# Performance work log

Measured on AMD Instinct MI355X. Metric: run time of the kernel, lower is better.

Reference implementation:

```python
import jax, jax.numpy as jnp
import numpy as np

S = 8192  # query length
T = 8192  # key/value length
D = 256   # head dim


def setup_inputs() -> dict:
    key = jax.random.key(0)
    kq, kk, kv = jax.random.split(key, 3)
    return {
        "query": jax.random.normal(kq, (S, D), dtype=jnp.float32),
        "key": jax.random.normal(kk, (T, D), dtype=jnp.float32),
        "value": jax.random.normal(kv, (T, D), dtype=jnp.float32),
    }


def reference(query, key, value):
    # attn_weights = Q @ K^T  (contract last dims, no batch dims)  -> [S, T]
    attn_weights = jnp.einsum("sd,td->st", query, key)
    # SoftmaxAttn: softmax over axes [ndim//2, ndim) == last axis for 2D
    attn_weights = jax.nn.softmax(attn_weights, axis=-1).astype(jnp.float32)
    # y = A @ V  -> [S, D]
    y = jnp.einsum("st,td->sd", attn_weights, value)
    return y
```

## Files before the change

kernel.cpp:

```cpp
#include <hip/hip_runtime.h>
#include <hip/hip_fp16.h>

#define S_LEN 8192
#define T_LEN 8192
#define D_DIM 256
#define QBLK 128
#define KVBLK 32
#define TSPLIT 8
#define NKV ((T_LEN / TSPLIT) / KVBLK)
#define NQT (S_LEN / QBLK)
#define KTILE_BYTES 16384
#define VTILE_BYTES 16384
#define RESCALE_THR 6.0f
#define LOG2E 1.44269504f
#define SMEM_BYTES 65536

typedef _Float16 f16x8 __attribute__((ext_vector_type(8)));
typedef float f32x4 __attribute__((ext_vector_type(4)));

struct h4 { _Float16 h[4]; };

#define GLOAD_LDS16(g, l)                                              \
    __builtin_amdgcn_global_load_lds(                                  \
        (const __attribute__((address_space(1))) void*)(g),            \
        (__attribute__((address_space(3))) void*)(l), 16, 0, 0)

#define MFMA16(a, b, c) __builtin_amdgcn_mfma_f32_16x16x32_f16(a, b, c, 0, 0, 0)

#if __has_builtin(__builtin_amdgcn_exp2f)
#define EXP2(x) __builtin_amdgcn_exp2f(x)
#else
static __device__ __forceinline__ float EXP2(float x) {
    float y;
    asm("v_exp_f32 %0, %1" : "=v"(y) : "v"(x));
    return y;
}
#endif

__global__ __launch_bounds__(256) void cvt_kernel(const float* __restrict__ in,
                                                  _Float16* __restrict__ out, int n4) {
    int i = blockIdx.x * 256 + threadIdx.x;
    if (i < n4) {
        float4 v = ((const float4*)in)[i];
        h4 o;
        o.h[0] = (_Float16)(v.x * LOG2E); o.h[1] = (_Float16)(v.y * LOG2E);
        o.h[2] = (_Float16)(v.z * LOG2E); o.h[3] = (_Float16)(v.w * LOG2E);
        ((h4*)out)[i] = o;
    }
}

__global__ __launch_bounds__(256) void cvt_swz_kernel(const float* __restrict__ in,
                                                      _Float16* __restrict__ img,
                                                      int nchunks) {
    int id = blockIdx.x * 256 + threadIdx.x;
    if (id >= nchunks) return;
    int row = id >> 5, gr = id & 31;
    int t = row >> 5, r = row & 31;
    float4 a = *(const float4*)(in + (size_t)row * D_DIM + gr * 8);
    float4 b = *(const float4*)(in + (size_t)row * D_DIM + gr * 8 + 4);
    f16x8 o;
    o[0] = (_Float16)a.x; o[1] = (_Float16)a.y; o[2] = (_Float16)a.z; o[3] = (_Float16)a.w;
    o[4] = (_Float16)b.x; o[5] = (_Float16)b.y; o[6] = (_Float16)b.z; o[7] = (_Float16)b.w;
    *(f16x8*)((char*)img + (size_t)t * KTILE_BYTES + (gr >> 2) * 2048 +
              ((r >> 4) << 10) + ((r & 15) << 6) + ((gr & 3) << 4)) = o;
}

__global__ __launch_bounds__(256) void vt_swz_kernel(const float* __restrict__ V,
                                                     _Float16* __restrict__ Vimg) {
    __shared__ float tile[32][260];
    const int t = blockIdx.x;
#pragma unroll
    for (int i = 0; i < 8; ++i) {
        int idx = i * 256 + threadIdx.x;
        int kr = idx >> 6, c4 = idx & 63;
        float4 v = *(const float4*)(V + ((size_t)t * 32 + kr) * D_DIM + c4 * 4);
        tile[kr][c4 * 4 + 0] = v.x;
        tile[kr][c4 * 4 + 1] = v.y;
        tile[kr][c4 * 4 + 2] = v.z;
        tile[kr][c4 * 4 + 3] = v.w;
    }
    __syncthreads();
#pragma unroll
    for (int i = 0; i < 4; ++i) {
        int gid = i * 256 + threadIdx.x;
        int d = gid >> 2, gk = gid & 3;
        f16x8 o;
#pragma unroll
        for (int j = 0; j < 8; ++j)
            o[j] = (_Float16)tile[(j >> 2) * 16 + gk * 4 + (j & 3)][d];
        *(f16x8*)((char*)Vimg + (size_t)t * VTILE_BYTES + ((d >> 4) << 10) +
                  (gk << 8) + ((d & 15) << 4)) = o;
    }
}

__global__ __launch_bounds__(256, 2) void attn_kernel(
    const _Float16* __restrict__ Qh, const _Float16* __restrict__ Kimg,
    const _Float16* __restrict__ Vimg, _Float16* __restrict__ Opart,
    float* __restrict__ ml) {
    extern __shared__ __align__(16) char smem[];
    char* sK = smem;
    char* sV = smem + 32768;
    const int tid = threadIdx.x;
    const int wave = tid >> 6, lane = tid & 63;
    const int g = lane >> 4, c = lane & 15;
    const int bid = blockIdx.x;
    const int qtile = bid >> 3, split = bid & 7;
    const int tile0 = split * NKV;
    const int rot = ((qtile >> 5) << 4) | ((qtile & 3) << 2);
    const int othr = tid * 16;
    const int kbase = ((lane & 15) << 6) | ((lane >> 4) << 4);
    const int vbase = lane << 4;

#define TILE_AT(k) (tile0 + (((k) + rot) & (NKV - 1)))
#define STAGE_KV(k, slot)                                                          \
    {                                                                              \
        const char* Kt = (const char*)Kimg + (size_t)TILE_AT(k) * KTILE_BYTES;     \
        const char* Vt = (const char*)Vimg + (size_t)TILE_AT(k) * VTILE_BYTES;     \
        _Pragma("unroll") for (int i = 0; i < 4; ++i) {                            \
            GLOAD_LDS16(Kt + i * 4096 + othr, sK + (slot)*16384 + i * 4096 + othr); \
            GLOAD_LDS16(Vt + i * 4096 + othr, sV + (slot)*16384 + i * 4096 + othr); \
        }                                                                          \
    }

    f16x8 qf[2][8];
    {
        const size_t qrow0 = (size_t)qtile * QBLK + wave * 32 + c;
#pragma unroll
        for (int mi = 0; mi < 2; ++mi)
#pragma unroll
            for (int ks = 0; ks < 8; ++ks)
                qf[mi][ks] =
                    *(const f16x8*)(Qh + (qrow0 + mi * 16) * D_DIM + (ks * 4 + g) * 8);
    }

    f32x4 acc[2][16];
#pragma unroll
    for (int mi = 0; mi < 2; ++mi)
#pragma unroll
        for (int dt = 0; dt < 16; ++dt) acc[mi][dt] = (f32x4){0.f, 0.f, 0.f, 0.f};
    float m[2] = {-1e30f, -1e30f};
    float l[2] = {0.f, 0.f};

    STAGE_KV(0, 0);

    for (int kt = 0; kt < NKV; ++kt) {
        asm volatile("s_waitcnt lgkmcnt(0)" ::: "memory");
        asm volatile("s_waitcnt vmcnt(0)" ::: "memory");
        __builtin_amdgcn_s_barrier();

        if (kt + 1 < NKV) STAGE_KV(kt + 1, (kt + 1) & 1);

        const char* sKb = sK + (kt & 1) * 16384;
        const char* sVb = sV + (kt & 1) * 16384;

        f32x4 st[2][2];
#pragma unroll
        for (int mi = 0; mi < 2; ++mi)
#pragma unroll
            for (int ct = 0; ct < 2; ++ct) st[mi][ct] = (f32x4){0.f, 0.f, 0.f, 0.f};
        __builtin_amdgcn_s_setprio(1);
#pragma unroll
        for (int ks = 0; ks < 8; ++ks) {
            f16x8 kf0 = *(const f16x8*)(sKb + ks * 2048 + kbase);
            f16x8 kf1 = *(const f16x8*)(sKb + ks * 2048 + 1024 + kbase);
            st[0][0] = MFMA16(kf0, qf[0][ks], st[0][0]);
            st[0][1] = MFMA16(kf1, qf[0][ks], st[0][1]);
            st[1][0] = MFMA16(kf0, qf[1][ks], st[1][0]);
            st[1][1] = MFMA16(kf1, qf[1][ks], st[1][1]);
        }
        __builtin_amdgcn_s_setprio(0);

        union PU { unsigned int u[4]; f16x8 v; };
        PU pu[2];
#pragma unroll
        for (int mi = 0; mi < 2; ++mi) {
            float pm = fmaxf(fmaxf(fmaxf(st[mi][0][0], st[mi][0][1]),
                                   fmaxf(st[mi][0][2], st[mi][0][3])),
                             fmaxf(fmaxf(st[mi][1][0], st[mi][1][1]),
                                   fmaxf(st[mi][1][2], st[mi][1][3])));
            if (__any(pm > m[mi] + RESCALE_THR)) {
                pm = fmaxf(pm, __shfl_xor(pm, 16));
                pm = fmaxf(pm, __shfl_xor(pm, 32));
                float mn = fmaxf(m[mi], pm);
                float sc = EXP2(m[mi] - mn);
                m[mi] = mn;
                l[mi] *= sc;
                float fr[4];
#pragma unroll
                for (int r = 0; r < 4; ++r) fr[r] = __shfl(sc, (g << 4) | (g * 4 + r));
#pragma unroll
                for (int dt = 0; dt < 16; ++dt)
#pragma unroll
                    for (int r = 0; r < 4; ++r) acc[mi][dt][r] *= fr[r];
            }
            float rs = 0.f;
#pragma unroll
            for (int ct = 0; ct < 2; ++ct)
#pragma unroll
                for (int r = 0; r < 4; ++r) {
                    float p = EXP2(st[mi][ct][r] - m[mi]);
                    st[mi][ct][r] = p;
                    rs += p;
                }
            l[mi] += rs;
            pu[mi].u[0] = __builtin_bit_cast(
                unsigned int, __builtin_amdgcn_cvt_pkrtz(st[mi][0][0], st[mi][0][1]));
            pu[mi].u[1] = __builtin_bit_cast(
                unsigned int, __builtin_amdgcn_cvt_pkrtz(st[mi][0][2], st[mi][0][3]));
            pu[mi].u[2] = __builtin_bit_cast(
                unsigned int, __builtin_amdgcn_cvt_pkrtz(st[mi][1][0], st[mi][1][1]));
            pu[mi].u[3] = __builtin_bit_cast(
                unsigned int, __builtin_amdgcn_cvt_pkrtz(st[mi][1][2], st[mi][1][3]));
        }

        __builtin_amdgcn_s_setprio(1);
#pragma unroll
        for (int dt = 0; dt < 16; ++dt) {
            f16x8 vf = *(const f16x8*)(sVb + dt * 1024 + vbase);
            acc[0][dt] = MFMA16(pu[0].v, vf, acc[0][dt]);
            acc[1][dt] = MFMA16(pu[1].v, vf, acc[1][dt]);
        }
        __builtin_amdgcn_s_setprio(0);
    }

    _Float16* Ob = Opart + (size_t)(qtile * TSPLIT + split) * QBLK * D_DIM;
#pragma unroll
    for (int mi = 0; mi < 2; ++mi)
#pragma unroll
        for (int dt = 0; dt < 16; ++dt)
#pragma unroll
            for (int r = 0; r < 4; ++r) {
                int row = wave * 32 + mi * 16 + g * 4 + r;
                int col = dt * 16 + c;
                Ob[(size_t)row * D_DIM + col] = (_Float16)acc[mi][dt][r];
            }
#pragma unroll
    for (int mi = 0; mi < 2; ++mi) {
        l[mi] += __shfl_xor(l[mi], 16);
        l[mi] += __shfl_xor(l[mi], 32);
    }
    if (g == 0) {
        float* mlb = ml + (size_t)((qtile * TSPLIT + split) * QBLK) * 2;
#pragma unroll
        for (int mi = 0; mi < 2; ++mi) {
            int row = wave * 32 + mi * 16 + c;
            mlb[row * 2 + 0] = m[mi];
            mlb[row * 2 + 1] = l[mi];
        }
    }
}

__global__ __launch_bounds__(256) void combine_kernel(const _Float16* __restrict__ Opart,
                                                      const float* __restrict__ ml,
                                                      float* __restrict__ out) {
    int r = blockIdx.x;
    int qtile = r >> 7, rl = r & 127;
    int d = threadIdx.x;
    float mv[TSPLIT], lv[TSPLIT];
    float M = -1e30f;
#pragma unroll
    for (int s = 0; s < TSPLIT; ++s) {
        const float* mlb = ml + (size_t)((qtile * TSPLIT + s) * QBLK + rl) * 2;
        mv[s] = mlb[0];
        lv[s] = mlb[1];
        M = fmaxf(M, mv[s]);
    }
    float num = 0.f, den = 0.f;
#pragma unroll
    for (int s = 0; s < TSPLIT; ++s) {
        float w = EXP2(mv[s] - M);
        num += w * (float)Opart[((size_t)(qtile * TSPLIT + s) * QBLK + rl) * D_DIM + d];
        den += w * lv[s];
    }
    out[(size_t)r * D_DIM + d] = num / den;
}

extern "C" void kernel_launch(void* const* d_in, const int* in_sizes, int n_in,
                              void* d_out, int out_size, void* d_ws, size_t ws_size,
                              hipStream_t stream) {
    const float* Q = (const float*)d_in[0];
    const float* K = (const float*)d_in[1];
    const float* V = (const float*)d_in[2];
    float* out = (float*)d_out;
    char* ws = (char*)d_ws;

    _Float16* Qh = (_Float16*)ws;
    _Float16* Kimg = (_Float16*)(ws + (4 << 20));
    _Float16* Vimg = (_Float16*)(ws + (8 << 20));
    _Float16* Opart = (_Float16*)(ws + (12 << 20));
    float* ml = (float*)(ws + ((size_t)44 << 20));

    const int n4 = S_LEN * D_DIM / 4;
    const int nchunks = S_LEN * D_DIM / 8;
    cvt_kernel<<<n4 / 256, 256, 0, stream>>>(Q, Qh, n4);
    cvt_swz_kernel<<<nchunks / 256, 256, 0, stream>>>(K, Kimg, nchunks);
    vt_swz_kernel<<<T_LEN / 32, 256, 0, stream>>>(V, Vimg);

    attn_kernel<<<NQT * TSPLIT, 256, SMEM_BYTES, stream>>>(Qh, Kimg, Vimg, Opart, ml);
    combine_kernel<<<S_LEN, 256, 0, stream>>>(Opart, ml, out);
}
```

Before: 103.3 us.

## Switch attention MFMAs from 16x16x32 to 32x32x16 with matching K/V swizzle

Recasts the QK^T and PV matrix products to use the 32x32x16 f16 MFMA instead of 16x16x32. The K and V preprocessing kernels now write tiles in the lane-linear order that instruction expects. Each wave now handles 32 query rows as a single softmax row group, with one running max and sum per lane. The goal is fewer MFMA issues and fewer LDS fragment loads per tile, plus less per-row bookkeeping. The cost is larger accumulator register tiles, a different rescale shuffle pattern, and two split accumulators in QK that must be added together.

```diff
diff --git a/kernel.cpp b/kernel.cpp
--- a/kernel.cpp
+++ b/kernel.cpp
@@ -16,7 +16,7 @@
 #define SMEM_BYTES 65536
 
 typedef _Float16 f16x8 __attribute__((ext_vector_type(8)));
-typedef float f32x4 __attribute__((ext_vector_type(4)));
+typedef float f32x16 __attribute__((ext_vector_type(16)));
 
 struct h4 { _Float16 h[4]; };
 
@@ -25,7 +25,7 @@
         (const __attribute__((address_space(1))) void*)(g),            \
         (__attribute__((address_space(3))) void*)(l), 16, 0, 0)
 
-#define MFMA16(a, b, c) __builtin_amdgcn_mfma_f32_16x16x32_f16(a, b, c, 0, 0, 0)
+#define MFMA32(a, b, c) __builtin_amdgcn_mfma_f32_32x32x16_f16(a, b, c, 0, 0, 0)
 
 #if __has_builtin(__builtin_amdgcn_exp2f)
 #define EXP2(x) __builtin_amdgcn_exp2f(x)
@@ -51,18 +51,19 @@
 
 __global__ __launch_bounds__(256) void cvt_swz_kernel(const float* __restrict__ in,
                                                       _Float16* __restrict__ img,
-                                                      int nchunks) {
+                                                      int ngran) {
     int id = blockIdx.x * 256 + threadIdx.x;
-    if (id >= nchunks) return;
-    int row = id >> 5, gr = id & 31;
-    int t = row >> 5, r = row & 31;
-    float4 a = *(const float4*)(in + (size_t)row * D_DIM + gr * 8);
-    float4 b = *(const float4*)(in + (size_t)row * D_DIM + gr * 8 + 4);
+    if (id >= ngran) return;
+    int t = id >> 10, g = id & 1023;
+    int s = g >> 6, l = g & 63;
+    int row = t * 32 + (l & 31);
+    int col = s * 16 + (l >> 5) * 8;
+    float4 a = *(const float4*)(in + (size_t)row * D_DIM + col);
+    float4 b = *(const float4*)(in + (size_t)row * D_DIM + col + 4);
     f16x8 o;
     o[0] = (_Float16)a.x; o[1] = (_Float16)a.y; o[2] = (_Float16)a.z; o[3] = (_Float16)a.w;
     o[4] = (_Float16)b.x; o[5] = (_Float16)b.y; o[6] = (_Float16)b.z; o[7] = (_Float16)b.w;
-    *(f16x8*)((char*)img + (size_t)t * KTILE_BYTES + (gr >> 2) * 2048 +
-              ((r >> 4) << 10) + ((r & 15) << 6) + ((gr & 3) << 4)) = o;
+    *(f16x8*)((char*)img + (size_t)id * 16) = o;
 }
 
 __global__ __launch_bounds__(256) void vt_swz_kernel(const float* __restrict__ V,
@@ -82,14 +83,14 @@
     __syncthreads();
 #pragma unroll
     for (int i = 0; i < 4; ++i) {
-        int gid = i * 256 + threadIdx.x;
-        int d = gid >> 2, gk = gid & 3;
+        int g = i * 256 + threadIdx.x;
+        int dt = g >> 7, s = (g >> 6) & 1, l = g & 63;
+        int hi = l >> 5, d = dt * 32 + (l & 31);
         f16x8 o;
 #pragma unroll
         for (int j = 0; j < 8; ++j)
-            o[j] = (_Float16)tile[(j >> 2) * 16 + gk * 4 + (j & 3)][d];
-        *(f16x8*)((char*)Vimg + (size_t)t * VTILE_BYTES + ((d >> 4) << 10) +
-                  (gk << 8) + ((d & 15) << 4)) = o;
+            o[j] = (_Float16)tile[16 * s + 4 * hi + 8 * (j >> 2) + (j & 3)][d];
+        *(f16x8*)((char*)Vimg + (size_t)t * VTILE_BYTES + (size_t)g * 16) = o;
     }
 }
 
@@ -102,14 +103,13 @@
     char* sV = smem + 32768;
     const int tid = threadIdx.x;
     const int wave = tid >> 6, lane = tid & 63;
-    const int g = lane >> 4, c = lane & 15;
+    const int q31 = lane & 31, hi = lane >> 5;
     const int bid = blockIdx.x;
     const int qtile = bid >> 3, split = bid & 7;
     const int tile0 = split * NKV;
     const int rot = ((qtile >> 5) << 4) | ((qtile & 3) << 2);
     const int othr = tid * 16;
-    const int kbase = ((lane & 15) << 6) | ((lane >> 4) << 4);
-    const int vbase = lane << 4;
+    const int lb = lane * 16;
 
 #define TILE_AT(k) (tile0 + (((k) + rot) & (NKV - 1)))
 #define STAGE_KV(k, slot)                                                          \
@@ -122,24 +122,21 @@
         }                                                                          \
     }
 
-    f16x8 qf[2][8];
+    f16x8 qf[16];
     {
-        const size_t qrow0 = (size_t)qtile * QBLK + wave * 32 + c;
-#pragma unroll
-        for (int mi = 0; mi < 2; ++mi)
-#pragma unroll
-            for (int ks = 0; ks < 8; ++ks)
-                qf[mi][ks] =
-                    *(const f16x8*)(Qh + (qrow0 + mi * 16) * D_DIM + (ks * 4 + g) * 8);
-    }
-
-    f32x4 acc[2][16];
-#pragma unroll
-    for (int mi = 0; mi < 2; ++mi)
-#pragma unroll
-        for (int dt = 0; dt < 16; ++dt) acc[mi][dt] = (f32x4){0.f, 0.f, 0.f, 0.f};
-    float m[2] = {-1e30f, -1e30f};
-    float l[2] = {0.f, 0.f};
+        const size_t qrow = (size_t)qtile * QBLK + wave * 32 + q31;
+#pragma unroll
+        for (int s = 0; s < 16; ++s)
+            qf[s] = *(const f16x8*)(Qh + qrow * D_DIM + s * 16 + hi * 8);
+    }
+
+    f32x16 acc[8];
+#pragma unroll
+    for (int dt = 0; dt < 8; ++dt)
+#pragma unroll
+        for (int r = 0; r < 16; ++r) acc[dt][r] = 0.f;
+    float m = -1e30f;
+    float l = 0.f;
 
     STAGE_KV(0, 0);
 
@@ -153,100 +150,84 @@
         const char* sKb = sK + (kt & 1) * 16384;
         const char* sVb = sV + (kt & 1) * 16384;
 
-        f32x4 st[2][2];
-#pragma unroll
-        for (int mi = 0; mi < 2; ++mi)
-#pragma unroll
-            for (int ct = 0; ct < 2; ++ct) st[mi][ct] = (f32x4){0.f, 0.f, 0.f, 0.f};
+        f32x16 sa, sb;
+#pragma unroll
+        for (int r = 0; r < 16; ++r) { sa[r] = 0.f; sb[r] = 0.f; }
         __builtin_amdgcn_s_setprio(1);
 #pragma unroll
-        for (int ks = 0; ks < 8; ++ks) {
-            f16x8 kf0 = *(const f16x8*)(sKb + ks * 2048 + kbase);
-            f16x8 kf1 = *(const f16x8*)(sKb + ks * 2048 + 1024 + kbase);
-            st[0][0] = MFMA16(kf0, qf[0][ks], st[0][0]);
-            st[0][1] = MFMA16(kf1, qf[0][ks], st[0][1]);
-            st[1][0] = MFMA16(kf0, qf[1][ks], st[1][0]);
-            st[1][1] = MFMA16(kf1, qf[1][ks], st[1][1]);
+        for (int s = 0; s < 16; s += 2) {
+            f16x8 kfa = *(const f16x8*)(sKb + s * 1024 + lb);
+            f16x8 kfb = *(const f16x8*)(sKb + (s + 1) * 1024 + lb);
+            sa = MFMA32(kfa, qf[s], sa);
+            sb = MFMA32(kfb, qf[s + 1], sb);
         }
         __builtin_amdgcn_s_setprio(0);
+        f32x16 st = sa + sb;
+
+        float pm = st[0];
+#pragma unroll
+        for (int r = 1; r < 16; ++r) pm = fmaxf(pm, st[r]);
+        pm = fmaxf(pm, __shfl_xor(pm, 32));
+        if (__any(pm > m + RESCALE_THR)) {
+            float mn = fmaxf(m, pm);
+            float sc = EXP2(m - mn);
+            m = mn;
+            l *= sc;
+            float fr[16];
+#pragma unroll
+            for (int r = 0; r < 16; ++r)
+                fr[r] = __shfl(sc, (r & 3) + 8 * (r >> 2) + 4 * hi);
+#pragma unroll
+            for (int dt = 0; dt < 8; ++dt)
+#pragma unroll
+                for (int r = 0; r < 16; ++r) acc[dt][r] *= fr[r];
+        }
+        float rs = 0.f;
+#pragma unroll
+        for (int r = 0; r < 16; ++r) {
+            float p = EXP2(st[r] - m);
+            st[r] = p;
+            rs += p;
+        }
+        l += rs;
 
         union PU { unsigned int u[4]; f16x8 v; };
-        PU pu[2];
-#pragma unroll
-        for (int mi = 0; mi < 2; ++mi) {
-            float pm = fmaxf(fmaxf(fmaxf(st[mi][0][0], st[mi][0][1]),
-                                   fmaxf(st[mi][0][2], st[mi][0][3])),
-                             fmaxf(fmaxf(st[mi][1][0], st[mi][1][1]),
-                                   fmaxf(st[mi][1][2], st[mi][1][3])));
-            if (__any(pm > m[mi] + RESCALE_THR)) {
-                pm = fmaxf(pm, __shfl_xor(pm, 16));
-                pm = fmaxf(pm, __shfl_xor(pm, 32));
-                float mn = fmaxf(m[mi], pm);
-                float sc = EXP2(m[mi] - mn);
-                m[mi] = mn;
-                l[mi] *= sc;
-                float fr[4];
-#pragma unroll
-                for (int r = 0; r < 4; ++r) fr[r] = __shfl(sc, (g << 4) | (g * 4 + r));
-#pragma unroll
-                for (int dt = 0; dt < 16; ++dt)
-#pragma unroll
-                    for (int r = 0; r < 4; ++r) acc[mi][dt][r] *= fr[r];
-            }
-            float rs = 0.f;
-#pragma unroll
-            for (int ct = 0; ct < 2; ++ct)
-#pragma unroll
-                for (int r = 0; r < 4; ++r) {
-                    float p = EXP2(st[mi][ct][r] - m[mi]);
-                    st[mi][ct][r] = p;
-                    rs += p;
-                }
-            l[mi] += rs;
-            pu[mi].u[0] = __builtin_bit_cast(
-                unsigned int, __builtin_amdgcn_cvt_pkrtz(st[mi][0][0], st[mi][0][1]));
-            pu[mi].u[1] = __builtin_bit_cast(
-                unsigned int, __builtin_amdgcn_cvt_pkrtz(st[mi][0][2], st[mi][0][3]));
-            pu[mi].u[2] = __builtin_bit_cast(
-                unsigned int, __builtin_amdgcn_cvt_pkrtz(st[mi][1][0], st[mi][1][1]));
-            pu[mi].u[3] = __builtin_bit_cast(
-                unsigned int, __builtin_amdgcn_cvt_pkrtz(st[mi][1][2], st[mi][1][3]));
+        PU pa0, pa1;
+#pragma unroll
+        for (int i = 0; i < 4; ++i) {
+            pa0.u[i] = __builtin_bit_cast(
+                unsigned int, __builtin_amdgcn_cvt_pkrtz(st[2 * i], st[2 * i + 1]));
+            pa1.u[i] = __builtin_bit_cast(
+                unsigned int, __builtin_amdgcn_cvt_pkrtz(st[8 + 2 * i], st[9 + 2 * i]));
         }
 
         __builtin_amdgcn_s_setprio(1);
 #pragma unroll
-        for (int dt = 0; dt < 16; ++dt) {
-            f16x8 vf = *(const f16x8*)(sVb + dt * 1024 + vbase);
-            acc[0][dt] = MFMA16(pu[0].v, vf, acc[0][dt]);
-            acc[1][dt] = MFMA16(pu[1].v, vf, acc[1][dt]);
+        for (int dt = 0; dt < 8; ++dt) {
+            f16x8 vf0 = *(const f16x8*)(sVb + dt * 2048 + lb);
+            f16x8 vf1 = *(const f16x8*)(sVb + dt * 2048 + 1024 + lb);
+            acc[dt] = MFMA32(pa0.v, vf0, acc[dt]);
+            acc[dt] = MFMA32(pa1.v, vf1, acc[dt]);
         }
         __builtin_amdgcn_s_setprio(0);
     }
 
     _Float16* Ob = Opart + (size_t)(qtile * TSPLIT + split) * QBLK * D_DIM;
 #pragma unroll
-    for (int mi = 0; mi < 2; ++mi)
-#pragma unroll
-        for (int dt = 0; dt < 16; ++dt)
-#pragma unroll
-            for (int r = 0; r < 4; ++r) {
-                int row = wave * 32 + mi * 16 + g * 4 + r;
-                int col = dt * 16 + c;
-                Ob[(size_t)row * D_DIM + col] = (_Float16)acc[mi][dt][r];
-            }
-#pragma unroll
-    for (int mi = 0; mi < 2; ++mi) {
-        l[mi] += __shfl_xor(l[mi], 16);
-        l[mi] += __shfl_xor(l[mi], 32);
-    }
-    if (g == 0) {
+    for (int dt = 0; dt < 8; ++dt)
+#pragma unroll
+        for (int r = 0; r < 16; ++r) {
+            int q = (r & 3) + 8 * (r >> 2) + 4 * hi;
+            int row = wave * 32 + q;
+            int col = dt * 32 + q31;
+            Ob[(size_t)row * D_DIM + col] = (_Float16)acc[dt][r];
+        }
+    l += __shfl_xor(l, 32);
+    if (lane < 32) {
         float* mlb = ml + (size_t)((qtile * TSPLIT + split) * QBLK) * 2;
-#pragma unroll
-        for (int mi = 0; mi < 2; ++mi) {
-            int row = wave * 32 + mi * 16 + c;
-            mlb[row * 2 + 0] = m[mi];
-            mlb[row * 2 + 1] = l[mi];
-        }
+        int row = wave * 32 + lane;
+        mlb[row * 2 + 0] = m;
+        mlb[row * 2 + 1] = l;
     }
 }
 
@@ -291,9 +272,9 @@
     float* ml = (float*)(ws + ((size_t)44 << 20));
 
     const int n4 = S_LEN * D_DIM / 4;
-    const int nchunks = S_LEN * D_DIM / 8;
+    const int ngran = S_LEN * D_DIM / 8;
     cvt_kernel<<<n4 / 256, 256, 0, stream>>>(Q, Qh, n4);
-    cvt_swz_kernel<<<nchunks / 256, 256, 0, stream>>>(K, Kimg, nchunks);
+    cvt_swz_kernel<<<ngran / 256, 256, 0, stream>>>(K, Kimg, ngran);
     vt_swz_kernel<<<T_LEN / 32, 256, 0, stream>>>(V, Vimg);
 
     attn_kernel<<<NQT * TSPLIT, 256, SMEM_BYTES, stream>>>(Qh, Kimg, Vimg, Opart, ml);
```

New measurement: 107.6 us. 1.04x slower.
